# Kernel tuning notes

Hardware: AMD Instinct MI355X
Metric: run time of the kernel (lower is better)

The kernel has to match this reference:

```python
import jax, jax.numpy as jnp
import numpy as np

N = 500_000
IN_CH = 64
OUT_CH = 32
HEADS = 4
NUM_SEGS = 1024


def setup_inputs() -> dict:
    key = jax.random.key(0)
    ks = jax.random.split(key, 8)
    x = jax.random.normal(ks[0], (N, IN_CH), dtype=jnp.float32)
    batch = jnp.sort(jax.random.randint(ks[1], (N,), 0, NUM_SEGS, dtype=jnp.int32))
    batch = batch.at[-1].set(NUM_SEGS - 1)  # mimic size = batch[-1]+1 == NUM_SEGS
    s_in = 1.0 / np.sqrt(IN_CH)
    s_hg = 1.0 / np.sqrt(HEADS * IN_CH)
    s_hm = 1.0 / np.sqrt(OUT_CH * HEADS)
    # gate_nn: Linear(in, heads*in, bias=False) -> PReLU -> Linear(heads*in, heads, bias=False)
    gate_w1 = jax.random.uniform(ks[2], (HEADS * IN_CH, IN_CH), jnp.float32, -s_in, s_in)
    prelu_a = jnp.asarray(0.25, dtype=jnp.float32)
    gate_w2 = jax.random.uniform(ks[3], (HEADS, HEADS * IN_CH), jnp.float32, -s_hg, s_hg)
    # nn: Linear(in, out*heads) -> ReLU -> Linear(out*heads, out*heads)
    mlp_w1 = jax.random.uniform(ks[4], (OUT_CH * HEADS, IN_CH), jnp.float32, -s_in, s_in)
    mlp_b1 = jax.random.uniform(ks[5], (OUT_CH * HEADS,), jnp.float32, -s_in, s_in)
    mlp_w2 = jax.random.uniform(ks[6], (OUT_CH * HEADS, OUT_CH * HEADS), jnp.float32, -s_hm, s_hm)
    mlp_b2 = jax.random.uniform(ks[7], (OUT_CH * HEADS,), jnp.float32, -s_hm, s_hm)
    return {"x": x, "batch": batch, "num_segments": NUM_SEGS,
            "gate_w1": gate_w1, "prelu_a": prelu_a, "gate_w2": gate_w2,
            "mlp_w1": mlp_w1, "mlp_b1": mlp_b1, "mlp_w2": mlp_w2, "mlp_b2": mlp_b2}


def reference(x, batch, num_segments, gate_w1, prelu_a, gate_w2,
              mlp_w1, mlp_b1, mlp_w2, mlp_b2):
    n = x.shape[0]
    # gate network: [N, heads]
    h = x @ gate_w1.T
    h = jnp.where(h >= 0, h, prelu_a * h)  # PReLU (shared scalar slope)
    gate = h @ gate_w2.T
    # feature MLP: [N, heads, out]
    feat = jax.nn.relu(x @ mlp_w1.T + mlp_b1) @ mlp_w2.T + mlp_b2
    feat = feat.reshape(n, HEADS, -1)
    # segment (per-graph) softmax over nodes, per head
    gmax = jax.ops.segment_max(gate, batch, num_segments=num_segments)  # [S, heads]
    escore = jnp.exp(gate - gmax[batch])
    denom = jax.ops.segment_sum(escore, batch, num_segments=num_segments)
    score = escore / (denom[batch] + 1e-16)  # [N, heads]
    # weighted scatter-add pooling
    out = jax.ops.segment_sum(score[..., None] * feat, batch, num_segments=num_segments)
    return out.reshape(num_segments, -1)  # [S, heads*out]
```

## Files before the change

kernel.cpp:

```cpp
#include <hip/hip_runtime.h>
#include <cstdint>
#include <cstddef>

#define NN 500000
#define NG 15625
#define NBLK 512
#define NWAVES (NBLK * 4)

typedef __attribute__((ext_vector_type(8))) short short8;
typedef __attribute__((ext_vector_type(4))) float floatx4;
typedef __attribute__((ext_vector_type(4))) float fv4;

__device__ __forceinline__ unsigned short f2bf(float f) {
  union { float f; unsigned u; } v; v.f = f;
  unsigned r = v.u + 0x7FFFu + ((v.u >> 16) & 1u);
  return (unsigned short)(r >> 16);
}
__device__ __forceinline__ unsigned cvtpk(float a, float b) {
  unsigned r;
  asm("v_cvt_pk_bf16_f32 %0, %1, %2" : "=v"(r) : "v"(a), "v"(b));
  return r;
}
__device__ __forceinline__ float bflo(unsigned u) {
  union { unsigned u; float f; } v; v.u = u << 16; return v.f;
}
__device__ __forceinline__ float bfhi(unsigned u) {
  union { unsigned u; float f; } v; v.u = u & 0xffff0000u; return v.f;
}

#define MFMA16(a, b, c) __builtin_amdgcn_mfma_f32_16x16x32_bf16((a), (b), (c), 0, 0, 0)

#define FLUSH() do {                                                          \
  if (quad == 0) {                                                            \
    _Pragma("unroll") for (int mt_ = 0; mt_ < 8; ++mt_)                       \
      _Pragma("unroll") for (int r_ = 0; r_ < 4; ++r_)                        \
        atomicAdd(&zws[((size_t)cur_seg * 4 + r_) * 128 + mt_ * 16 + lcol],   \
                  acc[mt_][r_]);                                              \
  }                                                                           \
  _Pragma("unroll") for (int mt_ = 0; mt_ < 8; ++mt_)                         \
    acc[mt_] = (floatx4){0.f, 0.f, 0.f, 0.f};                                 \
  { float v_ = es; v_ += __shfl_xor(v_, 16); v_ += __shfl_xor(v_, 32);        \
    if (lane < 4) atomicAdd(&denom[cur_seg * 4 + lane], v_); }                \
  es = 0.f;                                                                   \
} while (0)

__global__ __launch_bounds__(256, 2) void fused_kernel(
    const float* __restrict__ x, const int* __restrict__ batch,
    const float* __restrict__ gw1, const float* __restrict__ mw1,
    const float* __restrict__ gw2, const float* __restrict__ prelu_a,
    const float* __restrict__ b1, float* __restrict__ denom,
    float* __restrict__ zws) {
  __shared__ unsigned short wl[28672];
  const int t = threadIdx.x;

#pragma unroll 4
  for (int e = t; e < 28672; e += 256) {
    unsigned short v;
    if (e < 24576) {
      const float* src = (e < 16384) ? gw1 : mw1;
      int local = (e < 16384) ? e : e - 16384;
      int j = local & 7, lane = (local >> 3) & 63, tile = local >> 9;
      int row = (tile >> 1) * 16 + (lane & 15);
      int k = (tile & 1) * 32 + ((lane >> 4) & 3) * 8 + j;
      v = f2bf(src[row * 64 + k]);
    } else {
      int local = e - 24576;
      int j = local & 7, lane = (local >> 3) & 63, s = local >> 9;
      int row = lane & 15, q = (lane >> 4) & 3;
      int w = s * 32 + ((j >> 2) << 4) + 4 * q + (j & 3);
      v = (row < 4) ? f2bf(gw2[row * 256 + w]) : (unsigned short)0;
    }
    wl[e] = v;
  }
  __syncthreads();
  const unsigned short* gw1s = wl;
  const unsigned short* mw1s = wl + 16384;
  const unsigned short* gw2s = wl + 24576;

  const int wave = t >> 6, lane = t & 63;
  const int quad = lane >> 4, lcol = lane & 15;
  const float slope = prelu_a[0];
  const int W = blockIdx.x * 4 + wave;
  const int g0 = (int)(((long long)W * NG) / NWAVES);
  const int g1 = (int)(((long long)(W + 1) * NG) / NWAVES);

  float b1v[8];
#pragma unroll
  for (int mt = 0; mt < 8; ++mt) b1v[mt] = b1[mt * 16 + lcol];

  floatx4 acc[8];
#pragma unroll
  for (int mt = 0; mt < 8; ++mt) acc[mt] = (floatx4){0.f, 0.f, 0.f, 0.f};
  float es = 0.f;
  int fs = g0 * 32; if (fs > NN - 1) fs = NN - 1;
  int cur_seg = batch[fs];

  for (int g = g0; g < g1; ++g) {
    const int base = g * 32;
    int sv[2];
    short8 bx[2][2];
#pragma unroll
    for (int nt = 0; nt < 2; ++nt) {
      int node = base + nt * 16 + lcol;
      sv[nt] = batch[node];
      const float* xp = x + (size_t)node * 64 + quad * 8;
      fv4 v0 = *(const fv4*)xp,        v1 = *(const fv4*)(xp + 4);
      fv4 v2 = *(const fv4*)(xp + 32), v3 = *(const fv4*)(xp + 36);
      union { short8 s; unsigned u[4]; } u0, u1;
      u0.u[0] = cvtpk(v0[0], v0[1]); u0.u[1] = cvtpk(v0[2], v0[3]);
      u0.u[2] = cvtpk(v1[0], v1[1]); u0.u[3] = cvtpk(v1[2], v1[3]);
      u1.u[0] = cvtpk(v2[0], v2[1]); u1.u[1] = cvtpk(v2[2], v2[3]);
      u1.u[2] = cvtpk(v3[0], v3[1]); u1.u[3] = cvtpk(v3[2], v3[3]);
      bx[nt][0] = u0.s; bx[nt][1] = u1.s;
    }

    floatx4 cg0 = {0.f, 0.f, 0.f, 0.f}, cg1 = {0.f, 0.f, 0.f, 0.f};
#pragma unroll
    for (int sst = 0; sst < 8; ++sst) {
      union GB { short8 s; unsigned u[4]; } gb0, gb1;
#pragma unroll
      for (int half = 0; half < 2; ++half) {
        const int mt = sst * 2 + half;
        short8 a0 = *(const short8*)(gw1s + ((size_t)(mt * 2 + 0) * 64 + lane) * 8);
        short8 a1 = *(const short8*)(gw1s + ((size_t)(mt * 2 + 1) * 64 + lane) * 8);
        floatx4 c0 = {0.f, 0.f, 0.f, 0.f};
        c0 = MFMA16(a0, bx[0][0], c0);
        c0 = MFMA16(a1, bx[0][1], c0);
        floatx4 c1 = {0.f, 0.f, 0.f, 0.f};
        c1 = MFMA16(a0, bx[1][0], c1);
        c1 = MFMA16(a1, bx[1][1], c1);
        gb0.u[half * 2 + 0] = cvtpk(fmaxf(c0[0], slope * c0[0]),
                                    fmaxf(c0[1], slope * c0[1]));
        gb0.u[half * 2 + 1] = cvtpk(fmaxf(c0[2], slope * c0[2]),
                                    fmaxf(c0[3], slope * c0[3]));
        gb1.u[half * 2 + 0] = cvtpk(fmaxf(c1[0], slope * c1[0]),
                                    fmaxf(c1[1], slope * c1[1]));
        gb1.u[half * 2 + 1] = cvtpk(fmaxf(c1[2], slope * c1[2]),
                                    fmaxf(c1[3], slope * c1[3]));
      }
      short8 ga = *(const short8*)(gw2s + ((size_t)sst * 64 + lane) * 8);
      cg0 = MFMA16(ga, gb0.s, cg0);
      cg1 = MFMA16(ga, gb1.s, cg1);
    }
    float e0a[4], e1a[4];
#pragma unroll
    for (int hh = 0; hh < 4; ++hh) {
      e0a[hh] = __expf(cg0[hh]);
      e1a[hh] = __expf(cg1[hh]);
    }

    float ev[8]; int svb[8];
#pragma unroll
    for (int j = 0; j < 4; ++j) {
      int src = 4 * quad + j;
      svb[j]     = __shfl(sv[0], src);
      svb[4 + j] = __shfl(sv[1], src);
      float t0 = __shfl(e0a[0], src), t1 = __shfl(e0a[1], src);
      float t2 = __shfl(e0a[2], src), t3 = __shfl(e0a[3], src);
      float c01 = (lcol & 1) ? t1 : t0, c23 = (lcol & 1) ? t3 : t2;
      ev[j] = (lcol & 2) ? c23 : c01;
      t0 = __shfl(e1a[0], src); t1 = __shfl(e1a[1], src);
      t2 = __shfl(e1a[2], src); t3 = __shfl(e1a[3], src);
      c01 = (lcol & 1) ? t1 : t0; c23 = (lcol & 1) ? t3 : t2;
      ev[4 + j] = (lcol & 2) ? c23 : c01;
    }

    union BH { short8 s; unsigned u[4]; } zb[8];
#pragma unroll
    for (int mt = 0; mt < 8; ++mt) {
      short8 w0 = *(const short8*)(mw1s + ((size_t)(mt * 2 + 0) * 64 + lane) * 8);
      short8 w1 = *(const short8*)(mw1s + ((size_t)(mt * 2 + 1) * 64 + lane) * 8);
      float bb = b1v[mt];
      floatx4 c0 = {0.f, 0.f, 0.f, 0.f};
      c0 = MFMA16(bx[0][0], w0, c0);
      c0 = MFMA16(bx[0][1], w1, c0);
      floatx4 c1 = {0.f, 0.f, 0.f, 0.f};
      c1 = MFMA16(bx[1][0], w0, c1);
      c1 = MFMA16(bx[1][1], w1, c1);
      zb[mt].u[0] = cvtpk(fmaxf(c0[0] + bb, 0.f), fmaxf(c0[1] + bb, 0.f));
      zb[mt].u[1] = cvtpk(fmaxf(c0[2] + bb, 0.f), fmaxf(c0[3] + bb, 0.f));
      zb[mt].u[2] = cvtpk(fmaxf(c1[0] + bb, 0.f), fmaxf(c1[1] + bb, 0.f));
      zb[mt].u[3] = cvtpk(fmaxf(c1[2] + bb, 0.f), fmaxf(c1[3] + bb, 0.f));
    }

    int p = 0;
    while (p < 32) {
      int selv = (p >> 4) ? sv[1] : sv[0];
      int s = __shfl(selv, p & 15);
      if (s != cur_seg) { FLUSH(); cur_seg = s; }
      int cnt = (int)__popcll(__ballot(sv[0] == s)) +
                (int)__popcll(__ballot(sv[1] == s));
      union { unsigned u[4]; short8 s8; } ea;
#pragma unroll
      for (int jj = 0; jj < 4; ++jj) {
        float e0 = (lcol < 4 && svb[2 * jj] == s) ? ev[2 * jj] : 0.f;
        float e1 = (lcol < 4 && svb[2 * jj + 1] == s) ? ev[2 * jj + 1] : 0.f;
        ea.u[jj] = cvtpk(e0, e1);
        es += bflo(ea.u[jj]) + bfhi(ea.u[jj]);
      }
#pragma unroll
      for (int mt = 0; mt < 8; ++mt)
        acc[mt] = MFMA16(ea.s8, zb[mt].s, acc[mt]);
      p += (cnt >> 2);
    }
  }
  FLUSH();
}

__global__ __launch_bounds__(128) void finalize_kernel(
    const float* __restrict__ zws, const float* __restrict__ denom,
    const float* __restrict__ mw2, const float* __restrict__ b2,
    float* __restrict__ out) {
  __shared__ float zL[512];
  const int seg = blockIdx.x, t = threadIdx.x;
#pragma unroll
  for (int i = 0; i < 4; ++i) zL[t + i * 128] = zws[(size_t)seg * 512 + t + i * 128];
  __syncthreads();
  const int fcol = t, h = t >> 5;
  float d = denom[seg * 4 + h];
  const fv4* mrow = (const fv4*)(mw2 + (size_t)fcol * 128);
  const fv4* zrow = (const fv4*)(zL + h * 128);
  float a0 = 0.f, a1 = 0.f, a2 = 0.f, a3 = 0.f;
#pragma unroll 8
  for (int k = 0; k < 32; ++k) {
    fv4 w = mrow[k], z = zrow[k];
    a0 = fmaf(w[0], z[0], a0); a1 = fmaf(w[1], z[1], a1);
    a2 = fmaf(w[2], z[2], a2); a3 = fmaf(w[3], z[3], a3);
  }
  float acc = (a0 + a1) + (a2 + a3);
  out[(size_t)seg * 128 + fcol] = (d > 0.f) ? (acc / d + b2[fcol]) : 0.f;
}

extern "C" void kernel_launch(void* const* d_in, const int* in_sizes, int n_in,
                              void* d_out, int out_size, void* d_ws, size_t ws_size,
                              hipStream_t stream) {
  const float* x     = (const float*)d_in[0];
  const int*   batch = (const int*)d_in[1];
  const float* gw1 = (const float*)d_in[3];
  const float* pa  = (const float*)d_in[4];
  const float* gw2 = (const float*)d_in[5];
  const float* mw1 = (const float*)d_in[6];
  const float* mb1 = (const float*)d_in[7];
  const float* mw2 = (const float*)d_in[8];
  const float* mb2 = (const float*)d_in[9];
  float* out = (float*)d_out;

  char* ws = (char*)d_ws;
  float* denom = (float*)ws;
  float* zws   = (float*)(ws + 16384);

  hipMemsetAsync(denom, 0, 16384, stream);
  hipMemsetAsync(zws, 0, 2097152, stream);

  fused_kernel<<<NBLK, 256, 0, stream>>>(x, batch, gw1, mw1, gw2,
                                         pa, mb1, denom, zws);

  finalize_kernel<<<1024, 128, 0, stream>>>(zws, denom, mw2, mb2, out);
}
```

Before: 259.9 us.

## Prefetch next node group's x/batch, keep gate_w2 in registers, raise grid size

Software-pipelines the x and batch loads by issuing the next 32-node group's global loads before the current group's MFMA work, so memory latency overlaps compute. gate_w2 fragments now live in registers per lane instead of LDS, which shrinks shared memory and drops the per-iteration LDS reads. The grid grows from 512 to 768 blocks to add parallelism. The cost is higher register pressure from the prefetch buffers (32 floats) and 8 short8 fragments, which under launch_bounds(256,2) could cause spills. The prefetch also redundantly reloads the current group on the final iteration.

```diff
diff --git a/kernel.cpp b/kernel.cpp
--- a/kernel.cpp
+++ b/kernel.cpp
@@ -4,7 +4,7 @@
 
 #define NN 500000
 #define NG 15625
-#define NBLK 512
+#define NBLK 768
 #define NWAVES (NBLK * 4)
 
 typedef __attribute__((ext_vector_type(8))) short short8;
@@ -44,38 +44,36 @@
   es = 0.f;                                                                   \
 } while (0)
 
+#define PREF(gg) do {                                                         \
+  _Pragma("unroll") for (int nt_ = 0; nt_ < 2; ++nt_) {                       \
+    int node_ = (gg) * 32 + nt_ * 16 + lcol;                                  \
+    svp[nt_] = batch[node_];                                                  \
+    const float* xp_ = x + (size_t)node_ * 64 + quad * 8;                     \
+    xq[nt_][0] = *(const fv4*)xp_;        xq[nt_][1] = *(const fv4*)(xp_ + 4);\
+    xq[nt_][2] = *(const fv4*)(xp_ + 32); xq[nt_][3] = *(const fv4*)(xp_ + 36);\
+  } } while (0)
+
 __global__ __launch_bounds__(256, 2) void fused_kernel(
     const float* __restrict__ x, const int* __restrict__ batch,
     const float* __restrict__ gw1, const float* __restrict__ mw1,
     const float* __restrict__ gw2, const float* __restrict__ prelu_a,
     const float* __restrict__ b1, float* __restrict__ denom,
     float* __restrict__ zws) {
-  __shared__ unsigned short wl[28672];
+  __shared__ unsigned short wl[24576];
   const int t = threadIdx.x;
 
 #pragma unroll 4
-  for (int e = t; e < 28672; e += 256) {
-    unsigned short v;
-    if (e < 24576) {
-      const float* src = (e < 16384) ? gw1 : mw1;
-      int local = (e < 16384) ? e : e - 16384;
-      int j = local & 7, lane = (local >> 3) & 63, tile = local >> 9;
-      int row = (tile >> 1) * 16 + (lane & 15);
-      int k = (tile & 1) * 32 + ((lane >> 4) & 3) * 8 + j;
-      v = f2bf(src[row * 64 + k]);
-    } else {
-      int local = e - 24576;
-      int j = local & 7, lane = (local >> 3) & 63, s = local >> 9;
-      int row = lane & 15, q = (lane >> 4) & 3;
-      int w = s * 32 + ((j >> 2) << 4) + 4 * q + (j & 3);
-      v = (row < 4) ? f2bf(gw2[row * 256 + w]) : (unsigned short)0;
-    }
-    wl[e] = v;
+  for (int e = t; e < 24576; e += 256) {
+    const float* src = (e < 16384) ? gw1 : mw1;
+    int local = (e < 16384) ? e : e - 16384;
+    int j = local & 7, lane = (local >> 3) & 63, tile = local >> 9;
+    int row = (tile >> 1) * 16 + (lane & 15);
+    int k = (tile & 1) * 32 + ((lane >> 4) & 3) * 8 + j;
+    wl[e] = f2bf(src[row * 64 + k]);
   }
   __syncthreads();
   const unsigned short* gw1s = wl;
   const unsigned short* mw1s = wl + 16384;
-  const unsigned short* gw2s = wl + 24576;
 
   const int wave = t >> 6, lane = t & 63;
   const int quad = lane >> 4, lcol = lane & 15;
@@ -84,6 +82,18 @@
   const int g0 = (int)(((long long)W * NG) / NWAVES);
   const int g1 = (int)(((long long)(W + 1) * NG) / NWAVES);
 
+  short8 gareg[8];
+#pragma unroll
+  for (int sst = 0; sst < 8; ++sst) {
+    union { short8 s; unsigned short h[8]; } u;
+#pragma unroll
+    for (int j = 0; j < 8; ++j) {
+      int w = sst * 32 + ((j >> 2) << 4) + 4 * quad + (j & 3);
+      u.h[j] = (lcol < 4) ? f2bf(gw2[lcol * 256 + w]) : (unsigned short)0;
+    }
+    gareg[sst] = u.s;
+  }
+
   float b1v[8];
 #pragma unroll
   for (int mt = 0; mt < 8; ++mt) b1v[mt] = b1[mt * 16 + lcol];
@@ -95,23 +105,28 @@
   int fs = g0 * 32; if (fs > NN - 1) fs = NN - 1;
   int cur_seg = batch[fs];
 
+  int svp[2]; fv4 xq[2][4];
+  PREF(g0);
+
   for (int g = g0; g < g1; ++g) {
-    const int base = g * 32;
-    int sv[2];
+    int sv[2] = {svp[0], svp[1]};
     short8 bx[2][2];
 #pragma unroll
     for (int nt = 0; nt < 2; ++nt) {
-      int node = base + nt * 16 + lcol;
-      sv[nt] = batch[node];
-      const float* xp = x + (size_t)node * 64 + quad * 8;
-      fv4 v0 = *(const fv4*)xp,        v1 = *(const fv4*)(xp + 4);
-      fv4 v2 = *(const fv4*)(xp + 32), v3 = *(const fv4*)(xp + 36);
       union { short8 s; unsigned u[4]; } u0, u1;
-      u0.u[0] = cvtpk(v0[0], v0[1]); u0.u[1] = cvtpk(v0[2], v0[3]);
-      u0.u[2] = cvtpk(v1[0], v1[1]); u0.u[3] = cvtpk(v1[2], v1[3]);
-      u1.u[0] = cvtpk(v2[0], v2[1]); u1.u[1] = cvtpk(v2[2], v2[3]);
-      u1.u[2] = cvtpk(v3[0], v3[1]); u1.u[3] = cvtpk(v3[2], v3[3]);
+      u0.u[0] = cvtpk(xq[nt][0][0], xq[nt][0][1]);
+      u0.u[1] = cvtpk(xq[nt][0][2], xq[nt][0][3]);
+      u0.u[2] = cvtpk(xq[nt][1][0], xq[nt][1][1]);
+      u0.u[3] = cvtpk(xq[nt][1][2], xq[nt][1][3]);
+      u1.u[0] = cvtpk(xq[nt][2][0], xq[nt][2][1]);
+      u1.u[1] = cvtpk(xq[nt][2][2], xq[nt][2][3]);
+      u1.u[2] = cvtpk(xq[nt][3][0], xq[nt][3][1]);
+      u1.u[3] = cvtpk(xq[nt][3][2], xq[nt][3][3]);
       bx[nt][0] = u0.s; bx[nt][1] = u1.s;
+    }
+    {
+      int gn = (g + 1 < NG) ? (g + 1) : g;
+      PREF(gn);
     }
 
     floatx4 cg0 = {0.f, 0.f, 0.f, 0.f}, cg1 = {0.f, 0.f, 0.f, 0.f};
@@ -138,9 +153,8 @@
         gb1.u[half * 2 + 1] = cvtpk(fmaxf(c1[2], slope * c1[2]),
                                     fmaxf(c1[3], slope * c1[3]));
       }
-      short8 ga = *(const short8*)(gw2s + ((size_t)sst * 64 + lane) * 8);
-      cg0 = MFMA16(ga, gb0.s, cg0);
-      cg1 = MFMA16(ga, gb1.s, cg1);
+      cg0 = MFMA16(gareg[sst], gb0.s, cg0);
+      cg1 = MFMA16(gareg[sst], gb1.s, cg1);
     }
     float e0a[4], e1a[4];
 #pragma unroll
```

Result: no change. 257.3 us (-1.0%).
